# Kernel optimization log

Hardware: AMD Instinct MI355X
Metric: run time of the kernel (lower is better)

The kernel has to match this reference:

```python
import jax, jax.numpy as jnp
import numpy as np

INPUT_DIM = 512
HIDDEN_DIM = 1024
OUTPUT_DIM = 1000
BATCH = 256
SEQ_LEN = 256


def setup_inputs() -> dict:
    key = jax.random.key(0)
    ks = jax.random.split(key, 7)
    std = 1.0 / np.sqrt(HIDDEN_DIM)
    u = lambda k, shape: jax.random.uniform(k, shape, jnp.float32, -std, std)
    return {
        "x": jax.random.normal(ks[0], (BATCH, SEQ_LEN, INPUT_DIM), jnp.float32),
        "w_x2h": u(ks[1], (4 * HIDDEN_DIM, INPUT_DIM)),
        "b_x2h": u(ks[2], (4 * HIDDEN_DIM,)),
        "w_h2h": u(ks[3], (4 * HIDDEN_DIM, HIDDEN_DIM)),
        "b_h2h": u(ks[4], (4 * HIDDEN_DIM,)),
        "w_fc": u(ks[5], (OUTPUT_DIM, HIDDEN_DIM)),
        "b_fc": u(ks[6], (OUTPUT_DIM,)),
    }


def _lstm_last_hidden(x, w_x2h, b_x2h, w_h2h, b_h2h):
    B, T, D = x.shape
    H = w_h2h.shape[1]
    # Precompute input-to-hidden for all timesteps in one big GEMM: [B,T,4H]
    xg = jnp.einsum("btd,gd->btg", x, w_x2h) + b_x2h + b_h2h
    xg = jnp.swapaxes(xg, 0, 1)  # [T,B,4H] for scan

    def step(carry, xg_t):
        h, c = carry
        gates = xg_t + h @ w_h2h.T  # [B,4H]
        i, f, g, o = jnp.split(gates, 4, axis=1)
        i = jax.nn.sigmoid(i)
        f = jax.nn.sigmoid(f)
        g = jnp.tanh(g)
        o = jax.nn.sigmoid(o)
        c = c * f + i * g
        h = o * jnp.tanh(c)
        return (h, c), None

    h0 = jnp.zeros((B, H), x.dtype)
    c0 = jnp.zeros((B, H), x.dtype)
    (h_last, _), _ = jax.lax.scan(step, (h0, c0), xg)
    return h_last


def reference(x, w_x2h, b_x2h, w_h2h, b_h2h, w_fc, b_fc):
    h_last = _lstm_last_hidden(x, w_x2h, b_x2h, w_h2h, b_h2h)  # [B,H]
    return h_last @ w_fc.T + b_fc  # [B,OUTPUT_DIM]
```

## Files before the change

### kernel.cpp

```cpp
#include <hip/hip_runtime.h>

typedef __attribute__((ext_vector_type(8))) short short8;
typedef __attribute__((ext_vector_type(4))) float floatx4;

#define DIN  512
#define HSZ  1024
#define G4   4096
#define KTOT 1536
#define BQ   256
#define TT   256

#define MFMA __builtin_amdgcn_mfma_f32_16x16x32_bf16

__device__ __forceinline__ unsigned short f2bf(float f){
  unsigned int u = __float_as_uint(f);
  u += 0x7fffu + ((u >> 16) & 1u);
  return (unsigned short)(u >> 16);
}
__device__ __forceinline__ unsigned int pack2(float a, float b){
  return (unsigned int)f2bf(a) | ((unsigned int)f2bf(b) << 16);
}

__global__ void prep_wcat(const float* __restrict__ wx, const float* __restrict__ wh,
                          const float* __restrict__ bx, const float* __restrict__ bh,
                          unsigned short* __restrict__ Wcat, float* __restrict__ bias){
  int gid = blockIdx.x * blockDim.x + threadIdx.x;
  int idx = gid * 8;
  int g = idx / KTOT;
  int k = idx - g * KTOT;
  const float* src = (k < DIN) ? (wx + (size_t)g * DIN + k)
                               : (wh + (size_t)g * HSZ + (k - DIN));
  float4 f0 = *(const float4*)(src);
  float4 f1 = *(const float4*)(src + 4);
  uint4 v = make_uint4(pack2(f0.x,f0.y), pack2(f0.z,f0.w), pack2(f1.x,f1.y), pack2(f1.z,f1.w));
  *(uint4*)(Wcat + (size_t)g * KTOT + k) = v;
  if (gid < G4) bias[gid] = bx[gid] + bh[gid];
}

__global__ void prep_wfc(const float* __restrict__ wfc, unsigned short* __restrict__ Wfcb){
  int gid = blockIdx.x * blockDim.x + threadIdx.x;
  int idx = gid * 8;
  int n = idx >> 10;
  int k = idx & 1023;
  uint4 v;
  if (n < 1000){
    const float* src = wfc + (size_t)n * 1024 + k;
    float4 f0 = *(const float4*)(src);
    float4 f1 = *(const float4*)(src + 4);
    v = make_uint4(pack2(f0.x,f0.y), pack2(f0.z,f0.w), pack2(f1.x,f1.y), pack2(f1.z,f1.w));
  } else {
    v = make_uint4(0u, 0u, 0u, 0u);
  }
  *(uint4*)(Wfcb + idx) = v;
}

__global__ void prep_x(const float* __restrict__ x, unsigned short* __restrict__ xbf){
  int gid = blockIdx.x * 256 + threadIdx.x;
  int d8 = gid & 63;
  int b  = (gid >> 6) & 255;
  int t  = gid >> 14;
  const float* src = x + (((size_t)b * TT) + t) * DIN + d8 * 8;
  float4 f0 = *(const float4*)(src);
  float4 f1 = *(const float4*)(src + 4);
  uint4 v = make_uint4(pack2(f0.x,f0.y), pack2(f0.z,f0.w), pack2(f1.x,f1.y), pack2(f1.z,f1.w));
  *(uint4*)(xbf + (((size_t)t * BQ) + b) * DIN + d8 * 8) = v;
}

__global__ void init_misc(unsigned int* __restrict__ h0w, unsigned int* __restrict__ cnt, int ncnt){
  int gid = blockIdx.x * 256 + threadIdx.x;
  if (gid < 131072) h0w[gid] = 0u;
  if (gid < ncnt)   cnt[gid] = 0u;
}

__global__ __launch_bounds__(512, 2)
void lstm_persist(const unsigned short* __restrict__ xbf,
                  const unsigned short* __restrict__ Wcat,
                  const float* __restrict__ bias,
                  unsigned short* __restrict__ hseq,
                  unsigned int* __restrict__ cnt){
  extern __shared__ char smem[];
  char*  Ws  = smem;
  float* Gt2 = (float*)(smem + 98304);
  float* Bls = (float*)(smem + 98304 + 34816);

  const int tid  = threadIdx.x;
  const int bx   = blockIdx.x;
  const int bg   = bx >> 7;
  const int b0   = bg << 7;
  const int hb   = bx & 127;
  const int u0   = hb << 3;
  const int lane = tid & 63;
  const int w    = tid >> 6;
  const int rg   = w & 3;
  const int kg   = w >> 2;

  {
    int c  = tid >> 4;
    int ch = tid & 15;
    int g  = c >> 3, j = c & 7;
    const char* src = (const char*)(Wcat + (size_t)(g * HSZ + u0 + j) * KTOT);
    char* dst = Ws + c * 3072;
    int xr = j << 4;
    #pragma unroll
    for (int q = 0; q < 12; ++q){
      int k2 = ch * 192 + q * 16;
      *(uint4*)(dst + (k2 ^ xr)) = *(const uint4*)(src + k2);
    }
    if (tid < 32) Bls[tid] = bias[(size_t)(tid >> 3) * HSZ + u0 + (tid & 7)];
  }
  __syncthreads();

  const int kq8  = (lane >> 4) * 8;
  const int cA   = lane & 15;
  const int cB   = 16 + (lane & 15);
  const char* bpA = Ws + cA * 3072; const int xorA = (cA & 7) << 4;
  const char* bpB = Ws + cB * 3072; const int xorB = (cB & 7) << 4;

  const size_t rowA0 = (size_t)(b0 + rg * 32 + (lane & 15));

  const int erow = tid >> 2;
  const int eup  = (tid & 3) * 2;
  float cst0 = 0.f, cst1 = 0.f;

  for (int t = 0; t < TT; ++t){
    const unsigned short* hin  = hseq + (size_t)t * (BQ * HSZ);
    unsigned short*       hout = hseq + (size_t)(t + 1) * (BQ * HSZ);

    floatx4 acc[2][2][2];
    #pragma unroll
    for (int ab = 0; ab < 2; ++ab)
      #pragma unroll
      for (int rf = 0; rf < 2; ++rf)
        #pragma unroll
        for (int cf = 0; cf < 2; ++cf)
          acc[ab][rf][cf] = (floatx4){0.f,0.f,0.f,0.f};

    short8 X0[8], X1[8];
    {
      const unsigned short* xr0 = xbf + ((size_t)t * BQ + rowA0) * DIN + kg * 256 + kq8;
      const unsigned short* xr1 = xr0 + (size_t)16 * DIN;
      #pragma unroll
      for (int p = 0; p < 8; ++p){
        X0[p] = *(const short8*)(xr0 + p * 32);
        X1[p] = *(const short8*)(xr1 + p * 32);
      }
    }
    __builtin_amdgcn_sched_barrier(0);

    if (t > 0){
      if (tid < 64){
        const unsigned int* cp = &cnt[(((size_t)t * 2 + bg) * 8) * 16];
        const int g16 = (lane & 7) * 16;
        while (true){
          unsigned int v = __hip_atomic_load(cp + g16, __ATOMIC_RELAXED, __HIP_MEMORY_SCOPE_AGENT);
          if (__ballot(v >= 16u) == ~0ull) break;
          __builtin_amdgcn_s_sleep(1);
        }
      }
      __syncthreads();
      asm volatile("" ::: "memory");
    }

    {
      const int bbase = kg * 512 + kq8 * 2;
      short8 bA[2], bB[2];
      bA[0] = *(const short8*)(bpA + ((bbase     ) ^ xorA));
      bB[0] = *(const short8*)(bpB + ((bbase     ) ^ xorB));
      bA[1] = *(const short8*)(bpA + ((bbase + 64) ^ xorA));
      bB[1] = *(const short8*)(bpB + ((bbase + 64) ^ xorB));
      #pragma unroll
      for (int j = 0; j < 8; ++j){
        const int sl = j & 1;
        short8 b0 = bA[sl], b1 = bB[sl];
        if (j < 6){
          int bb = bbase + (j + 2) * 64;
          bA[sl] = *(const short8*)(bpA + (bb ^ xorA));
          bB[sl] = *(const short8*)(bpB + (bb ^ xorB));
        }
        acc[sl][0][0] = MFMA(X0[j], b0, acc[sl][0][0], 0, 0, 0);
        acc[sl][0][1] = MFMA(X0[j], b1, acc[sl][0][1], 0, 0, 0);
        acc[sl][1][0] = MFMA(X1[j], b0, acc[sl][1][0], 0, 0, 0);
        acc[sl][1][1] = MFMA(X1[j], b1, acc[sl][1][1], 0, 0, 0);
      }
    }

    {
      const unsigned short* hr0 = hin + rowA0 * HSZ + kg * 512 + kq8;
      const unsigned short* hr1 = hr0 + (size_t)16 * HSZ;
      short8 A0[16], A1[16];
      #pragma unroll
      for (int p = 0; p < 16; ++p){
        A0[p] = *(const short8*)(hr0 + p * 32);
        A1[p] = *(const short8*)(hr1 + p * 32);
      }
      __builtin_amdgcn_sched_barrier(0);
      const int bbase = 1024 + kg * 1024 + kq8 * 2;
      short8 bA[2], bB[2];
      bA[0] = *(const short8*)(bpA + ((bbase     ) ^ xorA));
      bB[0] = *(const short8*)(bpB + ((bbase     ) ^ xorB));
      bA[1] = *(const short8*)(bpA + ((bbase + 64) ^ xorA));
      bB[1] = *(const short8*)(bpB + ((bbase + 64) ^ xorB));
      #pragma unroll
      for (int j = 0; j < 16; ++j){
        const int sl = j & 1;
        short8 b0 = bA[sl], b1 = bB[sl];
        if (j < 14){
          int bb = bbase + (j + 2) * 64;
          bA[sl] = *(const short8*)(bpA + (bb ^ xorA));
          bB[sl] = *(const short8*)(bpB + (bb ^ xorB));
        }
        acc[sl][0][0] = MFMA(A0[j], b0, acc[sl][0][0], 0, 0, 0);
        acc[sl][0][1] = MFMA(A0[j], b1, acc[sl][0][1], 0, 0, 0);
        acc[sl][1][0] = MFMA(A1[j], b0, acc[sl][1][0], 0, 0, 0);
        acc[sl][1][1] = MFMA(A1[j], b1, acc[sl][1][1], 0, 0, 0);
      }
    }

    {
      float* gdst = Gt2 + kg * (128 * 34);
      int r0 = rg * 32 + (lane >> 4) * 4;
      #pragma unroll
      for (int rf = 0; rf < 2; ++rf){
        floatx4 g0 = acc[0][rf][0] + acc[1][rf][0];
        floatx4 g1 = acc[0][rf][1] + acc[1][rf][1];
        #pragma unroll
        for (int r = 0; r < 4; ++r){
          gdst[(r0 + rf * 16 + r) * 34 + cA] = g0[r];
          gdst[(r0 + rf * 16 + r) * 34 + cB] = g1[r];
        }
      }
    }
    __syncthreads();

    {
      const float* g0p = Gt2 + erow * 34;
      const float* g1p = g0p + 128 * 34;
      float gi0 = g0p[     eup] + g1p[     eup] + Bls[     eup];
      float gf0 = g0p[ 8 + eup] + g1p[ 8 + eup] + Bls[ 8 + eup];
      float gg0 = g0p[16 + eup] + g1p[16 + eup] + Bls[16 + eup];
      float go0 = g0p[24 + eup] + g1p[24 + eup] + Bls[24 + eup];
      float gi1 = g0p[     eup + 1] + g1p[     eup + 1] + Bls[     eup + 1];
      float gf1 = g0p[ 8 + eup + 1] + g1p[ 8 + eup + 1] + Bls[ 8 + eup + 1];
      float gg1 = g0p[16 + eup + 1] + g1p[16 + eup + 1] + Bls[16 + eup + 1];
      float go1 = g0p[24 + eup + 1] + g1p[24 + eup + 1] + Bls[24 + eup + 1];

      float iv0 = 1.f / (1.f + __expf(-gi0));
      float fv0 = 1.f / (1.f + __expf(-gf0));
      float e20 = __expf(-2.f * fmaxf(fminf(gg0, 30.f), -30.f));
      float gv0 = (1.f - e20) / (1.f + e20);
      float ov0 = 1.f / (1.f + __expf(-go0));
      float cn0 = cst0 * fv0 + iv0 * gv0;
      cst0 = cn0;
      float ec0 = __expf(-2.f * fmaxf(fminf(cn0, 30.f), -30.f));
      float hv0 = ov0 * (1.f - ec0) / (1.f + ec0);

      float iv1 = 1.f / (1.f + __expf(-gi1));
      float fv1 = 1.f / (1.f + __expf(-gf1));
      float e21 = __expf(-2.f * fmaxf(fminf(gg1, 30.f), -30.f));
      float gv1 = (1.f - e21) / (1.f + e21);
      float ov1 = 1.f / (1.f + __expf(-go1));
      float cn1 = cst1 * fv1 + iv1 * gv1;
      cst1 = cn1;
      float ec1 = __expf(-2.f * fmaxf(fminf(cn1, 30.f), -30.f));
      float hv1 = ov1 * (1.f - ec1) / (1.f + ec1);

      __hip_atomic_store((unsigned int*)(hout + (size_t)(b0 + erow) * HSZ + u0 + eup),
                         pack2(hv0, hv1), __ATOMIC_RELAXED, __HIP_MEMORY_SCOPE_AGENT);
    }
    __syncthreads();

    if (tid == 0){
      __hip_atomic_fetch_add(&cnt[(((size_t)(t + 1) * 2 + bg) * 8 + (hb >> 4)) * 16], 1u,
                             __ATOMIC_RELAXED, __HIP_MEMORY_SCOPE_AGENT);
    }
  }
}

__global__ __launch_bounds__(256, 1)
void fc_kernel(const unsigned short* __restrict__ h, const unsigned short* __restrict__ wfc,
               const float* __restrict__ bfc, float* __restrict__ out){
  int bx = blockIdx.x, tid = threadIdx.x;
  int wave = tid >> 6, lane = tid & 63;
  int row0 = (bx >> 4) * 64 + wave * 16;
  int col0 = (bx & 15) * 64;
  int lr = lane & 15, lk = (lane >> 4) * 8;
  floatx4 acc[4] = {{0.f,0.f,0.f,0.f},{0.f,0.f,0.f,0.f},{0.f,0.f,0.f,0.f},{0.f,0.f,0.f,0.f}};
  #pragma unroll 4
  for (int ks = 0; ks < 32; ++ks){
    int k = ks * 32 + lk;
    short8 a = *(const short8*)(h + (size_t)(row0 + lr) * 1024 + k);
    #pragma unroll
    for (int fj = 0; fj < 4; ++fj){
      short8 b = *(const short8*)(wfc + (size_t)(col0 + fj * 16 + lr) * 1024 + k);
      acc[fj] = MFMA(a, b, acc[fj], 0, 0, 0);
    }
  }
  #pragma unroll
  for (int fj = 0; fj < 4; ++fj){
    int col = col0 + fj * 16 + lr;
    if (col < 1000){
      #pragma unroll
      for (int r = 0; r < 4; ++r){
        int row = row0 + (lane >> 4) * 4 + r;
        out[(size_t)row * 1000 + col] = acc[fj][r] + bfc[col];
      }
    }
  }
}

extern "C" void kernel_launch(void* const* d_in, const int* in_sizes, int n_in,
                              void* d_out, int out_size, void* d_ws, size_t ws_size,
                              hipStream_t stream){
  const float* x    = (const float*)d_in[0];
  const float* wx2h = (const float*)d_in[1];
  const float* bx2h = (const float*)d_in[2];
  const float* wh2h = (const float*)d_in[3];
  const float* bh2h = (const float*)d_in[4];
  const float* wfc  = (const float*)d_in[5];
  const float* bfc  = (const float*)d_in[6];
  float* out = (float*)d_out;
  char* ws = (char*)d_ws;

  unsigned short* Wcat = (unsigned short*)(ws + 0);
  unsigned short* Wfcb = (unsigned short*)(ws + 12582912);
  float*          bias = (float*)         (ws + 14680064);
  unsigned short* xbf  = (unsigned short*)(ws + 14696448);
  unsigned short* hseq = (unsigned short*)(ws + 81805312);
  unsigned int*   cntb = (unsigned int*)  (ws + 216547328);

  (void)hipFuncSetAttribute((const void*)lstm_persist,
                            hipFuncAttributeMaxDynamicSharedMemorySize, 133376);

  hipLaunchKernelGGL(prep_wcat, dim3(3072), dim3(256), 0, stream, wx2h, wh2h, bx2h, bh2h, Wcat, bias);
  hipLaunchKernelGGL(prep_wfc,  dim3(512),  dim3(256), 0, stream, wfc, Wfcb);
  hipLaunchKernelGGL(prep_x,    dim3(16384),dim3(256), 0, stream, x, xbf);
  hipLaunchKernelGGL(init_misc, dim3(512),  dim3(256), 0, stream,
                     (unsigned int*)hseq, cntb, (int)(263168 / 4));

  hipLaunchKernelGGL(lstm_persist, dim3(256), dim3(512), 133376, stream,
                     xbf, Wcat, bias, hseq, cntb);

  hipLaunchKernelGGL(fc_kernel, dim3(64), dim3(256), 0, stream,
                     hseq + (size_t)256 * BQ * HSZ, Wfcb, bfc, out);
}
```

Before: 3.109 ms.

## Split K across block pairs with partial-sum exchange and per-block ready flags

Each persistent block now owns 16 hidden units (64 gate columns) and half of the concatenated K range, instead of 8 units over the full K. Paired blocks trade fp32 partial gate sums through a double-buffered global scratch buffer and pair flags. Each block then applies the cell update to half of the batch rows. Per-timestep counters are replaced by per-block monotonic timestep flags, and each block waits only on the 64 producer blocks covering its h slice. This halves shared-memory weight rows per block and gives more MFMA columns per wave, at the cost of an extra global round-trip and pairwise sync every step.

```diff
diff --git a/kernel.cpp b/kernel.cpp
--- a/kernel.cpp
+++ b/kernel.cpp
@@ -66,10 +66,10 @@
   *(uint4*)(xbf + (((size_t)t * BQ) + b) * DIN + d8 * 8) = v;
 }
 
-__global__ void init_misc(unsigned int* __restrict__ h0w, unsigned int* __restrict__ cnt, int ncnt){
+__global__ void init_misc(unsigned int* __restrict__ h0w, unsigned int* __restrict__ flags, int nflags){
   int gid = blockIdx.x * 256 + threadIdx.x;
   if (gid < 131072) h0w[gid] = 0u;
-  if (gid < ncnt)   cnt[gid] = 0u;
+  if (gid < nflags) flags[gid] = 0u;
 }
 
 __global__ __launch_bounds__(512, 2)
@@ -77,83 +77,88 @@
                   const unsigned short* __restrict__ Wcat,
                   const float* __restrict__ bias,
                   unsigned short* __restrict__ hseq,
-                  unsigned int* __restrict__ cnt){
+                  float* __restrict__ pbuf,
+                  unsigned int* __restrict__ hflags,
+                  unsigned int* __restrict__ pflags){
   extern __shared__ char smem[];
   char*  Ws  = smem;
-  float* Gt2 = (float*)(smem + 98304);
+  float* Gt  = (float*)(smem + 98304);
   float* Bls = (float*)(smem + 98304 + 34816);
 
   const int tid  = threadIdx.x;
   const int bx   = blockIdx.x;
   const int bg   = bx >> 7;
+  const int cg   = (bx & 127) >> 1;
+  const int kg   = bx & 1;
   const int b0   = bg << 7;
-  const int hb   = bx & 127;
-  const int u0   = hb << 3;
+  const int u0   = cg << 4;
   const int lane = tid & 63;
   const int w    = tid >> 6;
-  const int rg   = w & 3;
-  const int kg   = w >> 2;
+  const int rg   = w >> 1;
+  const int kgg  = w & 1;
 
   {
-    int c  = tid >> 4;
-    int ch = tid & 15;
-    int g  = c >> 3, j = c & 7;
-    const char* src = (const char*)(Wcat + (size_t)(g * HSZ + u0 + j) * KTOT);
-    char* dst = Ws + c * 3072;
-    int xr = j << 4;
+    int c  = tid >> 3;
+    int ch = tid & 7;
+    int grow = (c >> 4) * HSZ + u0 + (c & 15);
+    const char* src = (const char*)(Wcat + (size_t)grow * KTOT + kg * 768);
+    char* dst = Ws + c * 1536;
+    int xr = (c & 7) << 4;
     #pragma unroll
     for (int q = 0; q < 12; ++q){
       int k2 = ch * 192 + q * 16;
       *(uint4*)(dst + (k2 ^ xr)) = *(const uint4*)(src + k2);
     }
-    if (tid < 32) Bls[tid] = bias[(size_t)(tid >> 3) * HSZ + u0 + (tid & 7)];
+    if (tid < 64) Bls[tid] = bias[(size_t)(tid >> 4) * HSZ + u0 + (tid & 15)];
   }
   __syncthreads();
 
-  const int kq8  = (lane >> 4) * 8;
-  const int cA   = lane & 15;
-  const int cB   = 16 + (lane & 15);
-  const char* bpA = Ws + cA * 3072; const int xorA = (cA & 7) << 4;
-  const char* bpB = Ws + cB * 3072; const int xorB = (cB & 7) << 4;
-
-  const size_t rowA0 = (size_t)(b0 + rg * 32 + (lane & 15));
-
-  const int erow = tid >> 2;
-  const int eup  = (tid & 3) * 2;
+  const int kq8 = (lane >> 4) * 8;
+  const int cb  = lane & 15;
+  const char* bp[4]; int xr4[4];
+  #pragma unroll
+  for (int cf = 0; cf < 4; ++cf){
+    int c = cf * 16 + cb;
+    bp[cf]  = Ws + c * 1536;
+    xr4[cf] = (c & 7) << 4;
+  }
+
+  const int kstart = kg * 768 + kgg * 384;
+  const int nx = (kstart < 512) ? (((512 - kstart) + 31) >> 5) : 0;
+  const size_t rowA = (size_t)(b0 + rg * 32 + (lane & 15));
+
+  const int erl = kg * 64 + (tid >> 3);
+  const int eup = (tid & 7) * 2;
   float cst0 = 0.f, cst1 = 0.f;
 
   for (int t = 0; t < TT; ++t){
     const unsigned short* hin  = hseq + (size_t)t * (BQ * HSZ);
     unsigned short*       hout = hseq + (size_t)(t + 1) * (BQ * HSZ);
 
-    floatx4 acc[2][2][2];
-    #pragma unroll
-    for (int ab = 0; ab < 2; ++ab)
-      #pragma unroll
-      for (int rf = 0; rf < 2; ++rf)
-        #pragma unroll
-        for (int cf = 0; cf < 2; ++cf)
-          acc[ab][rf][cf] = (floatx4){0.f,0.f,0.f,0.f};
-
-    short8 X0[8], X1[8];
-    {
-      const unsigned short* xr0 = xbf + ((size_t)t * BQ + rowA0) * DIN + kg * 256 + kq8;
-      const unsigned short* xr1 = xr0 + (size_t)16 * DIN;
-      #pragma unroll
-      for (int p = 0; p < 8; ++p){
-        X0[p] = *(const short8*)(xr0 + p * 32);
-        X1[p] = *(const short8*)(xr1 + p * 32);
+    short8 A0[12], A1[12];
+    {
+      const unsigned short* xr0 = xbf + ((size_t)t * BQ + rowA) * DIN + kq8;
+      const unsigned short* xr1 = xr0 + 16 * DIN;
+      #pragma unroll
+      for (int p = 0; p < 12; ++p){
+        if (p < nx){
+          int kgl = kstart + p * 32;
+          A0[p] = *(const short8*)(xr0 + kgl);
+          A1[p] = *(const short8*)(xr1 + kgl);
+        }
       }
     }
     __builtin_amdgcn_sched_barrier(0);
 
     if (t > 0){
       if (tid < 64){
-        const unsigned int* cp = &cnt[(((size_t)t * 2 + bg) * 8) * 16];
-        const int g16 = (lane & 7) * 16;
+        const unsigned int* base = hflags + (bg << 7);
+        int i1 = (kg == 0) ? (lane & 31) : (32 + lane);
+        int i2 = (kg == 0) ? (lane & 31) : (96 + (lane & 31));
         while (true){
-          unsigned int v = __hip_atomic_load(cp + g16, __ATOMIC_RELAXED, __HIP_MEMORY_SCOPE_AGENT);
-          if (__ballot(v >= 16u) == ~0ull) break;
+          unsigned int v1 = __hip_atomic_load(base + i1, __ATOMIC_RELAXED, __HIP_MEMORY_SCOPE_AGENT);
+          unsigned int v2 = __hip_atomic_load(base + i2, __ATOMIC_RELAXED, __HIP_MEMORY_SCOPE_AGENT);
+          if (__ballot(v1 >= (unsigned)t && v2 >= (unsigned)t) == ~0ull) break;
           __builtin_amdgcn_s_sleep(1);
         }
       }
@@ -162,87 +167,122 @@
     }
 
     {
-      const int bbase = kg * 512 + kq8 * 2;
-      short8 bA[2], bB[2];
-      bA[0] = *(const short8*)(bpA + ((bbase     ) ^ xorA));
-      bB[0] = *(const short8*)(bpB + ((bbase     ) ^ xorB));
-      bA[1] = *(const short8*)(bpA + ((bbase + 64) ^ xorA));
-      bB[1] = *(const short8*)(bpB + ((bbase + 64) ^ xorB));
-      #pragma unroll
-      for (int j = 0; j < 8; ++j){
-        const int sl = j & 1;
-        short8 b0 = bA[sl], b1 = bB[sl];
-        if (j < 6){
-          int bb = bbase + (j + 2) * 64;
-          bA[sl] = *(const short8*)(bpA + (bb ^ xorA));
-          bB[sl] = *(const short8*)(bpB + (bb ^ xorB));
+      const unsigned short* hr0 = hin + rowA * HSZ + kq8;
+      const unsigned short* hr1 = hr0 + 16 * HSZ;
+      #pragma unroll
+      for (int p = 0; p < 12; ++p){
+        if (p >= nx){
+          int hu = kstart + p * 32 - 512;
+          A0[p] = *(const short8*)(hr0 + hu);
+          A1[p] = *(const short8*)(hr1 + hu);
         }
-        acc[sl][0][0] = MFMA(X0[j], b0, acc[sl][0][0], 0, 0, 0);
-        acc[sl][0][1] = MFMA(X0[j], b1, acc[sl][0][1], 0, 0, 0);
-        acc[sl][1][0] = MFMA(X1[j], b0, acc[sl][1][0], 0, 0, 0);
-        acc[sl][1][1] = MFMA(X1[j], b1, acc[sl][1][1], 0, 0, 0);
-      }
-    }
-
-    {
-      const unsigned short* hr0 = hin + rowA0 * HSZ + kg * 512 + kq8;
-      const unsigned short* hr1 = hr0 + (size_t)16 * HSZ;
-      short8 A0[16], A1[16];
-      #pragma unroll
-      for (int p = 0; p < 16; ++p){
-        A0[p] = *(const short8*)(hr0 + p * 32);
-        A1[p] = *(const short8*)(hr1 + p * 32);
-      }
-      __builtin_amdgcn_sched_barrier(0);
-      const int bbase = 1024 + kg * 1024 + kq8 * 2;
-      short8 bA[2], bB[2];
-      bA[0] = *(const short8*)(bpA + ((bbase     ) ^ xorA));
-      bB[0] = *(const short8*)(bpB + ((bbase     ) ^ xorB));
-      bA[1] = *(const short8*)(bpA + ((bbase + 64) ^ xorA));
-      bB[1] = *(const short8*)(bpB + ((bbase + 64) ^ xorB));
-      #pragma unroll
-      for (int j = 0; j < 16; ++j){
-        const int sl = j & 1;
-        short8 b0 = bA[sl], b1 = bB[sl];
-        if (j < 14){
-          int bb = bbase + (j + 2) * 64;
-          bA[sl] = *(const short8*)(bpA + (bb ^ xorA));
-          bB[sl] = *(const short8*)(bpB + (bb ^ xorB));
+      }
+    }
+    __builtin_amdgcn_sched_barrier(0);
+
+    floatx4 acc[2][4];
+    #pragma unroll
+    for (int rf = 0; rf < 2; ++rf)
+      #pragma unroll
+      for (int cf = 0; cf < 4; ++cf)
+        acc[rf][cf] = (floatx4){0.f,0.f,0.f,0.f};
+    {
+      const int kOff = kgg * 768 + kq8 * 2;
+      short8 Bv[4][2];
+      #pragma unroll
+      for (int cf = 0; cf < 4; ++cf){
+        Bv[cf][0] = *(const short8*)(bp[cf] + ((kOff     ) ^ xr4[cf]));
+        Bv[cf][1] = *(const short8*)(bp[cf] + ((kOff + 64) ^ xr4[cf]));
+      }
+      #pragma unroll
+      for (int p = 0; p < 12; ++p){
+        const int sl = p & 1;
+        short8 b0v = Bv[0][sl], b1v = Bv[1][sl], b2v = Bv[2][sl], b3v = Bv[3][sl];
+        if (p < 10){
+          int ko = kOff + (p + 2) * 64;
+          #pragma unroll
+          for (int cf = 0; cf < 4; ++cf)
+            Bv[cf][sl] = *(const short8*)(bp[cf] + (ko ^ xr4[cf]));
         }
-        acc[sl][0][0] = MFMA(A0[j], b0, acc[sl][0][0], 0, 0, 0);
-        acc[sl][0][1] = MFMA(A0[j], b1, acc[sl][0][1], 0, 0, 0);
-        acc[sl][1][0] = MFMA(A1[j], b0, acc[sl][1][0], 0, 0, 0);
-        acc[sl][1][1] = MFMA(A1[j], b1, acc[sl][1][1], 0, 0, 0);
-      }
-    }
-
-    {
-      float* gdst = Gt2 + kg * (128 * 34);
+        acc[0][0] = MFMA(A0[p], b0v, acc[0][0], 0, 0, 0);
+        acc[0][1] = MFMA(A0[p], b1v, acc[0][1], 0, 0, 0);
+        acc[0][2] = MFMA(A0[p], b2v, acc[0][2], 0, 0, 0);
+        acc[0][3] = MFMA(A0[p], b3v, acc[0][3], 0, 0, 0);
+        acc[1][0] = MFMA(A1[p], b0v, acc[1][0], 0, 0, 0);
+        acc[1][1] = MFMA(A1[p], b1v, acc[1][1], 0, 0, 0);
+        acc[1][2] = MFMA(A1[p], b2v, acc[1][2], 0, 0, 0);
+        acc[1][3] = MFMA(A1[p], b3v, acc[1][3], 0, 0, 0);
+      }
+    }
+
+    {
       int r0 = rg * 32 + (lane >> 4) * 4;
-      #pragma unroll
-      for (int rf = 0; rf < 2; ++rf){
-        floatx4 g0 = acc[0][rf][0] + acc[1][rf][0];
-        floatx4 g1 = acc[0][rf][1] + acc[1][rf][1];
+      if (kgg == 0){
         #pragma unroll
-        for (int r = 0; r < 4; ++r){
-          gdst[(r0 + rf * 16 + r) * 34 + cA] = g0[r];
-          gdst[(r0 + rf * 16 + r) * 34 + cB] = g1[r];
-        }
-      }
+        for (int rf = 0; rf < 2; ++rf)
+          #pragma unroll
+          for (int cf = 0; cf < 4; ++cf)
+            #pragma unroll
+            for (int r = 0; r < 4; ++r)
+              Gt[(r0 + rf * 16 + r) * 68 + cf * 16 + cb] = acc[rf][cf][r];
+      }
+      __syncthreads();
+      if (kgg == 1){
+        #pragma unroll
+        for (int rf = 0; rf < 2; ++rf)
+          #pragma unroll
+          for (int cf = 0; cf < 4; ++cf)
+            #pragma unroll
+            for (int r = 0; r < 4; ++r)
+              Gt[(r0 + rf * 16 + r) * 68 + cf * 16 + cb] += acc[rf][cf][r];
+      }
+      __syncthreads();
+    }
+
+    {
+      int r  = tid >> 3;
+      int c8 = (tid & 7) * 8;
+      const unsigned long long* s64 =
+          (const unsigned long long*)&Gt[((1 - kg) * 64 + r) * 68 + c8];
+      unsigned long long* dst =
+          (unsigned long long*)(pbuf + (((size_t)(t & 1) * 256 + bx) * 4096) + r * 64 + c8);
+      #pragma unroll
+      for (int j = 0; j < 4; ++j)
+        __hip_atomic_store(dst + j, s64[j], __ATOMIC_RELAXED, __HIP_MEMORY_SCOPE_AGENT);
     }
     __syncthreads();
-
-    {
-      const float* g0p = Gt2 + erow * 34;
-      const float* g1p = g0p + 128 * 34;
-      float gi0 = g0p[     eup] + g1p[     eup] + Bls[     eup];
-      float gf0 = g0p[ 8 + eup] + g1p[ 8 + eup] + Bls[ 8 + eup];
-      float gg0 = g0p[16 + eup] + g1p[16 + eup] + Bls[16 + eup];
-      float go0 = g0p[24 + eup] + g1p[24 + eup] + Bls[24 + eup];
-      float gi1 = g0p[     eup + 1] + g1p[     eup + 1] + Bls[     eup + 1];
-      float gf1 = g0p[ 8 + eup + 1] + g1p[ 8 + eup + 1] + Bls[ 8 + eup + 1];
-      float gg1 = g0p[16 + eup + 1] + g1p[16 + eup + 1] + Bls[16 + eup + 1];
-      float go1 = g0p[24 + eup + 1] + g1p[24 + eup + 1] + Bls[24 + eup + 1];
+    if (tid == 0){
+      __hip_atomic_store(&pflags[bx], (unsigned)(t + 1), __ATOMIC_RELAXED, __HIP_MEMORY_SCOPE_AGENT);
+      while (__hip_atomic_load(&pflags[bx ^ 1], __ATOMIC_RELAXED, __HIP_MEMORY_SCOPE_AGENT) < (unsigned)(t + 1))
+        __builtin_amdgcn_s_sleep(1);
+    }
+    __syncthreads();
+    {
+      int r  = tid >> 3;
+      int c8 = (tid & 7) * 8;
+      const unsigned long long* src =
+          (const unsigned long long*)(pbuf + (((size_t)(t & 1) * 256 + (bx ^ 1)) * 4096) + r * 64 + c8);
+      float* gd = &Gt[(kg * 64 + r) * 68 + c8];
+      #pragma unroll
+      for (int j = 0; j < 4; ++j){
+        unsigned long long v = __hip_atomic_load(src + j, __ATOMIC_RELAXED, __HIP_MEMORY_SCOPE_AGENT);
+        union { unsigned long long q; float f[2]; } uu; uu.q = v;
+        gd[2 * j]     += uu.f[0];
+        gd[2 * j + 1] += uu.f[1];
+      }
+    }
+    __syncthreads();
+
+    {
+      const float* gr = &Gt[erl * 68];
+      float gi0 = gr[     eup] + Bls[     eup];
+      float gf0 = gr[16 + eup] + Bls[16 + eup];
+      float gg0 = gr[32 + eup] + Bls[32 + eup];
+      float go0 = gr[48 + eup] + Bls[48 + eup];
+      float gi1 = gr[     eup + 1] + Bls[     eup + 1];
+      float gf1 = gr[16 + eup + 1] + Bls[16 + eup + 1];
+      float gg1 = gr[32 + eup + 1] + Bls[32 + eup + 1];
+      float go1 = gr[48 + eup + 1] + Bls[48 + eup + 1];
 
       float iv0 = 1.f / (1.f + __expf(-gi0));
       float fv0 = 1.f / (1.f + __expf(-gf0));
@@ -264,15 +304,13 @@
       float ec1 = __expf(-2.f * fmaxf(fminf(cn1, 30.f), -30.f));
       float hv1 = ov1 * (1.f - ec1) / (1.f + ec1);
 
-      __hip_atomic_store((unsigned int*)(hout + (size_t)(b0 + erow) * HSZ + u0 + eup),
+      __hip_atomic_store((unsigned int*)(hout + (size_t)(b0 + erl) * HSZ + u0 + eup),
                          pack2(hv0, hv1), __ATOMIC_RELAXED, __HIP_MEMORY_SCOPE_AGENT);
     }
     __syncthreads();
 
-    if (tid == 0){
-      __hip_atomic_fetch_add(&cnt[(((size_t)(t + 1) * 2 + bg) * 8 + (hb >> 4)) * 16], 1u,
-                             __ATOMIC_RELAXED, __HIP_MEMORY_SCOPE_AGENT);
-    }
+    if (tid == 0)
+      __hip_atomic_store(&hflags[bx], (unsigned)(t + 1), __ATOMIC_RELAXED, __HIP_MEMORY_SCOPE_AGENT);
   }
 }
 
@@ -321,24 +359,26 @@
   float* out = (float*)d_out;
   char* ws = (char*)d_ws;
 
-  unsigned short* Wcat = (unsigned short*)(ws + 0);
-  unsigned short* Wfcb = (unsigned short*)(ws + 12582912);
-  float*          bias = (float*)         (ws + 14680064);
-  unsigned short* xbf  = (unsigned short*)(ws + 14696448);
-  unsigned short* hseq = (unsigned short*)(ws + 81805312);
-  unsigned int*   cntb = (unsigned int*)  (ws + 216547328);
+  unsigned short* Wcat   = (unsigned short*)(ws + 0);
+  unsigned short* Wfcb   = (unsigned short*)(ws + 12582912);
+  float*          bias   = (float*)         (ws + 14680064);
+  unsigned short* xbf    = (unsigned short*)(ws + 14696448);
+  unsigned short* hseq   = (unsigned short*)(ws + 81805312);
+  float*          pbuf   = (float*)         (ws + 216547328);
+  unsigned int*   hflags = (unsigned int*)  (ws + 224935936);
+  unsigned int*   pflags = (unsigned int*)  (ws + 224936960);
 
   (void)hipFuncSetAttribute((const void*)lstm_persist,
-                            hipFuncAttributeMaxDynamicSharedMemorySize, 133376);
+                            hipFuncAttributeMaxDynamicSharedMemorySize, 133632);
 
   hipLaunchKernelGGL(prep_wcat, dim3(3072), dim3(256), 0, stream, wx2h, wh2h, bx2h, bh2h, Wcat, bias);
   hipLaunchKernelGGL(prep_wfc,  dim3(512),  dim3(256), 0, stream, wfc, Wfcb);
   hipLaunchKernelGGL(prep_x,    dim3(16384),dim3(256), 0, stream, x, xbf);
   hipLaunchKernelGGL(init_misc, dim3(512),  dim3(256), 0, stream,
-                     (unsigned int*)hseq, cntb, (int)(263168 / 4));
-
-  hipLaunchKernelGGL(lstm_persist, dim3(256), dim3(512), 133376, stream,
-                     xbf, Wcat, bias, hseq, cntb);
+                     (unsigned int*)hseq, hflags, 512);
+
+  hipLaunchKernelGGL(lstm_persist, dim3(256), dim3(512), 133632, stream,
+                     xbf, Wcat, bias, hseq, pbuf, hflags, pflags);
 
   hipLaunchKernelGGL(fc_kernel, dim3(64), dim3(256), 0, stream,
                      hseq + (size_t)256 * BQ * HSZ, Wfcb, bfc, out);
```

New measurement: 3.547 ms. 14.1% more time.
